# Kernel optimization log

Measured on AMD Instinct MI355X. Metric: run time of the kernel, lower is better.

## Reference

```python
import jax, jax.numpy as jnp
import numpy as np

STATE_LEN = 256
EPS = 1e-5


def _ln(x, g, b):
    m = jnp.mean(x, axis=-1, keepdims=True)
    v = jnp.mean((x - m) ** 2, axis=-1, keepdims=True)
    return (x - m) / jnp.sqrt(v + EPS) * g + b


def setup_inputs() -> dict:
    key = jax.random.key(0)
    ks = jax.random.split(key, 12)
    B, S, L, D, DK, DV = 2, 256, 2048, 512, 64, 64
    T = L + 2 * S  # 2560
    def w(k, i, o):
        return jax.random.normal(k, (i, o), jnp.float32) * 0.02
    return {
        "x": jax.random.normal(ks[0], (B, T, D), jnp.float32),
        "w_q": w(ks[1], D, DK), "w_k": w(ks[2], D, DK), "w_v": w(ks[3], D, DV),
        "w_q_ss": w(ks[4], D, DK), "w_k_ss": w(ks[5], D, DK), "w_v_ss": w(ks[6], D, DV),
        "w_q_se": w(ks[7], D, DK), "w_k_se": w(ks[8], D, DK), "w_v_se": w(ks[9], D, DV),
        "ln_g": jnp.ones((D,), jnp.float32), "ln_b": jnp.zeros((D,), jnp.float32),
        "ln_g_ss": jnp.ones((D,), jnp.float32), "ln_b_ss": jnp.zeros((D,), jnp.float32),
        "ln_g_se": jnp.ones((D,), jnp.float32), "ln_b_se": jnp.zeros((D,), jnp.float32),
        "cope_emb": jax.random.normal(ks[10], (1, DK, T), jnp.float32),
    }


def reference(x, w_q, w_k, w_v, w_q_ss, w_k_ss, w_v_ss, w_q_se, w_k_se, w_v_se,
              ln_g, ln_b, ln_g_ss, ln_b_ss, ln_g_se, ln_b_se, cope_emb):
    S = STATE_LEN
    T = x.shape[1]
    # extract_state: [state_start | main | state_end]
    xs, xm, xe = x[:, :S], x[:, S:T - S], x[:, T - S:]
    xm = _ln(xm, ln_g, ln_b)
    xs = _ln(xs, ln_g_ss, ln_b_ss)
    xe = _ln(xe, ln_g_se, ln_b_se)
    q = jnp.concatenate([xs @ w_q_ss, xm @ w_q, xe @ w_q_se], axis=1)  # [B,T,DK]
    k = jnp.concatenate([xs @ w_k_ss, xm @ w_k, xe @ w_k_se], axis=1)
    v = jnp.concatenate([xs @ w_v_ss, xm @ w_v, xe @ w_v_se], axis=1)
    dk = q.shape[-1]
    # --- CoPE bias ---
    logits = jnp.einsum('btd,bsd->bts', q, k)  # [B,T,T]
    gates = jax.nn.sigmoid(logits)
    # reverse cumsum along keys (flip-cumsum-flip)
    pos = jnp.flip(jnp.cumsum(jnp.flip(gates, -1), axis=-1), -1)
    pos = jnp.minimum(pos, jnp.float32(T - 1))
    pf = jnp.floor(pos)
    pc = jnp.ceil(pos)
    li = jnp.einsum('btd,dm->btm', q, cope_emb[0])  # [B,T,T]
    lc = jnp.take_along_axis(li, pc.astype(jnp.int32), axis=-1)
    lf = jnp.take_along_axis(li, pf.astype(jnp.int32), axis=-1)
    w = pos - pf
    bias = lc * w + lf * (1.0 - w)
    # --- attention with tril-log mask + CoPE bias ---
    causal = jnp.tril(jnp.ones((T, T), dtype=bool))
    att_logits = logits / jnp.sqrt(jnp.float32(dk)) + jnp.where(causal, bias, -jnp.inf)
    attn = jax.nn.softmax(att_logits, axis=-1)
    return jnp.einsum('bts,bsd->btd', attn, v)
```

## Files before the change

### kernel.cpp

```cpp
#include <hip/hip_runtime.h>
#include <hip/hip_bf16.h>
#include <math.h>

using short8 = __attribute__((ext_vector_type(8))) short;
using f32x4  = __attribute__((ext_vector_type(4))) float;

constexpr int S_LEN  = 256;
constexpr int T      = 2560;
constexpr int D_IN   = 512;
constexpr int DK     = 64;
constexpr int B_N    = 2;
constexpr int SS     = 8;

__global__ __launch_bounds__(256) void lnprep_kernel(
    const float* __restrict__ x,
    const float* __restrict__ g_m,  const float* __restrict__ b_m,
    const float* __restrict__ g_s,  const float* __restrict__ b_s,
    const float* __restrict__ g_e,  const float* __restrict__ b_e,
    const float* __restrict__ w_qs, const float* __restrict__ w_ks, const float* __restrict__ w_vs,
    const float* __restrict__ w_q,  const float* __restrict__ w_k,  const float* __restrict__ w_v,
    const float* __restrict__ w_qe, const float* __restrict__ w_ke, const float* __restrict__ w_ve,
    const float* __restrict__ cope,
    __hip_bfloat16* __restrict__ xnh, __hip_bfloat16* __restrict__ xnl,
    __hip_bfloat16* __restrict__ wth, __hip_bfloat16* __restrict__ wtl,
    __hip_bfloat16* __restrict__ copeT)
{
    constexpr int LN_BLOCKS = (B_N * T) / 4;
    if (blockIdx.x < LN_BLOCKS) {
        const int wv   = threadIdx.x >> 6;
        const int lane = threadIdx.x & 63;
        const int row  = blockIdx.x * 4 + wv;
        const int t    = row % T;

        const float *gv, *bv;
        if (t < S_LEN)          { gv = g_s; bv = b_s; }
        else if (t < T - S_LEN) { gv = g_m; bv = b_m; }
        else                    { gv = g_e; bv = b_e; }

        const float4* xr4 = (const float4*)(x + (size_t)row * D_IN);
        float4 a = xr4[lane * 2], b4 = xr4[lane * 2 + 1];
        float xv[8] = {a.x, a.y, a.z, a.w, b4.x, b4.y, b4.z, b4.w};

        float s = 0.f;
#pragma unroll
        for (int j = 0; j < 8; ++j) s += xv[j];
#pragma unroll
        for (int off = 32; off > 0; off >>= 1) s += __shfl_down(s, off);
        s = __shfl(s, 0);
        const float mean = s * (1.0f / D_IN);

        float sq = 0.f;
#pragma unroll
        for (int j = 0; j < 8; ++j) { float d = xv[j] - mean; sq += d * d; }
#pragma unroll
        for (int off = 32; off > 0; off >>= 1) sq += __shfl_down(sq, off);
        sq = __shfl(sq, 0);
        const float inv = rsqrtf(sq * (1.0f / D_IN) + 1e-5f);

        const float4* gv4 = (const float4*)gv;
        const float4* bv4 = (const float4*)bv;
        float4 ga = gv4[lane * 2], gb = gv4[lane * 2 + 1];
        float4 ba = bv4[lane * 2], bb = bv4[lane * 2 + 1];
        float g8[8] = {ga.x, ga.y, ga.z, ga.w, gb.x, gb.y, gb.z, gb.w};
        float b8[8] = {ba.x, ba.y, ba.z, ba.w, bb.x, bb.y, bb.z, bb.w};

        short hs[8], ls[8];
#pragma unroll
        for (int j = 0; j < 8; ++j) {
            float v = (xv[j] - mean) * inv * g8[j] + b8[j];
            __hip_bfloat16 h  = __float2bfloat16(v);
            __hip_bfloat16 lo = __float2bfloat16(v - __bfloat162float(h));
            hs[j] = *(short*)&h;
            ls[j] = *(short*)&lo;
        }
        short8 H = {hs[0],hs[1],hs[2],hs[3],hs[4],hs[5],hs[6],hs[7]};
        short8 L = {ls[0],ls[1],ls[2],ls[3],ls[4],ls[5],ls[6],ls[7]};
        *(short8*)(xnh + (size_t)row * D_IN + lane * 8) = H;
        *(short8*)(xnl + (size_t)row * D_IN + lane * 8) = L;
        return;
    }

    const int i = (blockIdx.x - LN_BLOCKS) * 256 + threadIdx.x;
    constexpr int NW = 9 * DK * D_IN;
    if (i < NW) {
        const int matIdx = i >> 15;
        const int rem = i & 32767;
        const int col = rem >> 9, k = rem & 511;
        const float* W =
            (matIdx == 0) ? w_qs : (matIdx == 1) ? w_ks : (matIdx == 2) ? w_vs :
            (matIdx == 3) ? w_q  : (matIdx == 4) ? w_k  : (matIdx == 5) ? w_v  :
            (matIdx == 6) ? w_qe : (matIdx == 7) ? w_ke : w_ve;
        float f = W[(size_t)k * DK + col];
        __hip_bfloat16 h = __float2bfloat16(f);
        wth[i] = h;
        wtl[i] = __float2bfloat16(f - __bfloat162float(h));
    } else if (i < NW + T * DK) {
        const int j = i - NW;
        const int m = j >> 6, d = j & 63;
        copeT[j] = __float2bfloat16(cope[(size_t)d * T + m]);
    }
}

__global__ __launch_bounds__(256) void qkv_gemm_kernel(
    const __hip_bfloat16* __restrict__ xnh, const __hip_bfloat16* __restrict__ xnl,
    const __hip_bfloat16* __restrict__ wth, const __hip_bfloat16* __restrict__ wtl,
    __hip_bfloat16* __restrict__ qh, __hip_bfloat16* __restrict__ ql,
    __hip_bfloat16* __restrict__ kh, __hip_bfloat16* __restrict__ kl,
    __hip_bfloat16* __restrict__ vT)
{
    const int bid = blockIdx.x;
    const int mt = bid / 3, mat = bid % 3;
    const int r0 = mt * 64;
    const int b  = r0 / T, t0 = r0 % T;
    const int region = (t0 < S_LEN) ? 0 : (t0 < T - S_LEN) ? 1 : 2;
    const int matIdx = region * 3 + mat;

    const int tid = threadIdx.x, lane = tid & 63, wid = tid >> 6;
    const int wm = wid >> 1, wn = wid & 1;
    const int fr = lane & 15, k8 = (lane >> 4) * 8;

    f32x4 acc[2][2];
#pragma unroll
    for (int mf = 0; mf < 2; ++mf)
#pragma unroll
        for (int nf = 0; nf < 2; ++nf) acc[mf][nf] = (f32x4){0.f, 0.f, 0.f, 0.f};

    for (int ks = 0; ks < D_IN / 32; ++ks) {
        const int k = ks * 32 + k8;
        short8 ah[2], al[2], bh2[2], bl2[2];
#pragma unroll
        for (int mf = 0; mf < 2; ++mf) {
            size_t off = (size_t)(r0 + wm * 32 + mf * 16 + fr) * D_IN + k;
            ah[mf] = *(const short8*)(xnh + off);
            al[mf] = *(const short8*)(xnl + off);
        }
#pragma unroll
        for (int nf = 0; nf < 2; ++nf) {
            size_t off = ((size_t)matIdx * DK + wn * 32 + nf * 16 + fr) * D_IN + k;
            bh2[nf] = *(const short8*)(wth + off);
            bl2[nf] = *(const short8*)(wtl + off);
        }
#pragma unroll
        for (int mf = 0; mf < 2; ++mf)
#pragma unroll
            for (int nf = 0; nf < 2; ++nf) {
                acc[mf][nf] = __builtin_amdgcn_mfma_f32_16x16x32_bf16(ah[mf], bh2[nf], acc[mf][nf], 0, 0, 0);
                acc[mf][nf] = __builtin_amdgcn_mfma_f32_16x16x32_bf16(ah[mf], bl2[nf], acc[mf][nf], 0, 0, 0);
                acc[mf][nf] = __builtin_amdgcn_mfma_f32_16x16x32_bf16(al[mf], bh2[nf], acc[mf][nf], 0, 0, 0);
            }
    }

    const int r4 = (lane >> 4) * 4;
#pragma unroll
    for (int mf = 0; mf < 2; ++mf)
#pragma unroll
        for (int nf = 0; nf < 2; ++nf) {
            const int cg = wn * 32 + nf * 16 + fr;
#pragma unroll
            for (int j = 0; j < 4; ++j) {
                const int rg = r0 + wm * 32 + mf * 16 + r4 + j;
                float f = acc[mf][nf][j];
                __hip_bfloat16 h  = __float2bfloat16(f);
                __hip_bfloat16 lo = __float2bfloat16(f - __bfloat162float(h));
                if (mat == 0)      { qh[(size_t)rg * DK + cg] = h; ql[(size_t)rg * DK + cg] = lo; }
                else if (mat == 1) { kh[(size_t)rg * DK + cg] = h; kl[(size_t)rg * DK + cg] = lo; }
                else               { vT[((size_t)b * DK + cg) * T + (rg % T)] = h; }
            }
        }
}

__global__ __launch_bounds__(256) void gemm1_kernel(
    const __hip_bfloat16* __restrict__ qh, const __hip_bfloat16* __restrict__ ql,
    const __hip_bfloat16* __restrict__ kh, const __hip_bfloat16* __restrict__ kl,
    const __hip_bfloat16* __restrict__ copeT,
    float* __restrict__ logc, __hip_bfloat16* __restrict__ lic,
    int b0, int t_off, int TC)
{
    constexpr int TS = T / 64;
    const int per_b = (TC / 128) * TS;
    const int bb  = blockIdx.x / per_b;
    const int rem = blockIdx.x % per_b;
    const int ti  = rem / TS, si = rem % TS;
    const int t0  = ti * 128, s0 = si * 64;
    const int b   = b0 + bb;
    float*          logits_c = logc + (size_t)bb * TC * T;
    __hip_bfloat16* li_c     = lic  + (size_t)bb * TC * T;

    const int tid = threadIdx.x, lane = tid & 63, wid = tid >> 6;
    const int wm  = wid >> 1, wn = wid & 1;
    const int fr  = lane & 15, k8 = (lane >> 4) * 8;
    const size_t qb = (size_t)b * T * DK;

    short8 ah[4][2], al[4][2];
#pragma unroll
    for (int mf = 0; mf < 4; ++mf)
#pragma unroll
        for (int ks = 0; ks < 2; ++ks) {
            size_t off = qb + (size_t)(t_off + t0 + wm * 64 + mf * 16 + fr) * DK + ks * 32 + k8;
            ah[mf][ks] = *(const short8*)(qh + off);
            al[mf][ks] = *(const short8*)(ql + off);
        }
    short8 bh[2][2], bl[2][2], bc[2][2];
#pragma unroll
    for (int nf = 0; nf < 2; ++nf)
#pragma unroll
        for (int ks = 0; ks < 2; ++ks) {
            size_t off = (size_t)(s0 + wn * 32 + nf * 16 + fr) * DK + ks * 32 + k8;
            bh[nf][ks] = *(const short8*)(kh + qb + off);
            bl[nf][ks] = *(const short8*)(kl + qb + off);
            bc[nf][ks] = *(const short8*)(copeT + off);
        }

    f32x4 accL[4][2], accM[4][2];
#pragma unroll
    for (int mf = 0; mf < 4; ++mf)
#pragma unroll
        for (int nf = 0; nf < 2; ++nf) {
            accL[mf][nf] = (f32x4){0.f, 0.f, 0.f, 0.f};
            accM[mf][nf] = (f32x4){0.f, 0.f, 0.f, 0.f};
        }

#pragma unroll
    for (int mf = 0; mf < 4; ++mf)
#pragma unroll
        for (int nf = 0; nf < 2; ++nf)
#pragma unroll
            for (int ks = 0; ks < 2; ++ks) {
                accL[mf][nf] = __builtin_amdgcn_mfma_f32_16x16x32_bf16(ah[mf][ks], bh[nf][ks], accL[mf][nf], 0, 0, 0);
                accL[mf][nf] = __builtin_amdgcn_mfma_f32_16x16x32_bf16(ah[mf][ks], bl[nf][ks], accL[mf][nf], 0, 0, 0);
                accL[mf][nf] = __builtin_amdgcn_mfma_f32_16x16x32_bf16(al[mf][ks], bh[nf][ks], accL[mf][nf], 0, 0, 0);
                accM[mf][nf] = __builtin_amdgcn_mfma_f32_16x16x32_bf16(ah[mf][ks], bc[nf][ks], accM[mf][nf], 0, 0, 0);
            }

    const int r4 = (lane >> 4) * 4;
#pragma unroll
    for (int mf = 0; mf < 4; ++mf)
#pragma unroll
        for (int nf = 0; nf < 2; ++nf) {
            const int cg = s0 + wn * 32 + nf * 16 + fr;
#pragma unroll
            for (int j = 0; j < 4; ++j) {
                const int rl = t0 + wm * 64 + mf * 16 + r4 + j;
                const size_t o = (size_t)rl * T + cg;
                logits_c[o] = accL[mf][nf][j];
                li_c[o]     = __float2bfloat16(accM[mf][nf][j]);
            }
        }
}

__global__ __launch_bounds__(256) void phase2_kernel(
    const float* __restrict__ logc, __hip_bfloat16* __restrict__ lic,
    int t_off, int TC)
{
    constexpr int CH = T / 256;
    const int tid  = threadIdx.x;
    const int lane = tid & 63;
    const int wv   = tid >> 6;
    const int bb   = blockIdx.x / TC;
    const int rl   = blockIdx.x % TC;
    const int t    = t_off + rl;

    __shared__ __hip_bfloat16 sli[T];
    __shared__ float redS[4], redM[4], redE[4];

    const float*    lrow  = logc + ((size_t)bb * TC + rl) * T;
    __hip_bfloat16* lirow = lic  + ((size_t)bb * TC + rl) * T;

#pragma unroll
    for (int i = 0; i < 5; ++i) {
        const int idx = i * 256 + tid;
        ((unsigned int*)sli)[idx] = ((const unsigned int*)lirow)[idx];
    }

    const int s0 = tid * CH;
    float lg[CH], g[CH];
    float lsum = 0.f;
    const float2* lr2 = (const float2*)(lrow + s0);
#pragma unroll
    for (int i = 0; i < 5; ++i) {
        float2 v = lr2[i];
        lg[2 * i] = v.x; lg[2 * i + 1] = v.y;
    }
#pragma unroll
    for (int i = 0; i < CH; ++i) {
        g[i] = 1.0f / (1.0f + __expf(-lg[i]));
        lsum += g[i];
    }

    float incl = lsum;
#pragma unroll
    for (int off = 1; off < 64; off <<= 1) {
        float n = __shfl_up(incl, off);
        if (lane >= off) incl += n;
    }
    if (lane == 63) redS[wv] = incl;
    __syncthreads();
    float total = 0.f, wpre = 0.f;
#pragma unroll
    for (int w2 = 0; w2 < 4; ++w2) {
        float tw = redS[w2];
        total += tw;
        if (w2 < wv) wpre += tw;
    }
    float run = wpre + incl - lsum;

    float att[CH];
    float lmax = -INFINITY;
#pragma unroll
    for (int i = 0; i < CH; ++i) {
        int s = s0 + i;
        float pos = total - run;
        run += g[i];
        pos = fminf(pos, (float)(T - 1));
        float pf = floorf(pos);
        float w  = pos - pf;
        int ipf  = (int)pf;
        int ipc  = (int)ceilf(pos);
        float bias = __bfloat162float(sli[ipc]) * w
                   + __bfloat162float(sli[ipf]) * (1.0f - w);
        float al = lg[i] * 0.125f + bias;
        if (s > t) al = -INFINITY;
        att[i] = al;
        lmax = fmaxf(lmax, al);
    }

#pragma unroll
    for (int off = 32; off > 0; off >>= 1) lmax = fmaxf(lmax, __shfl_down(lmax, off));
    if (lane == 0) redM[wv] = lmax;
    __syncthreads();
    const float bmax = fmaxf(fmaxf(redM[0], redM[1]), fmaxf(redM[2], redM[3]));

    float e[CH];
    float esum = 0.f;
#pragma unroll
    for (int i = 0; i < CH; ++i) {
        e[i] = __expf(att[i] - bmax);
        esum += e[i];
    }
#pragma unroll
    for (int off = 32; off > 0; off >>= 1) esum += __shfl_down(esum, off);
    if (lane == 0) redE[wv] = esum;
    __syncthreads();
    const float rden = 1.0f / (redE[0] + redE[1] + redE[2] + redE[3]);

    unsigned int pw[5];
#pragma unroll
    for (int i = 0; i < 5; ++i) {
        __hip_bfloat16 p0 = __float2bfloat16(e[2 * i] * rden);
        __hip_bfloat16 p1 = __float2bfloat16(e[2 * i + 1] * rden);
        pw[i] = (unsigned int)*(unsigned short*)&p0
              | ((unsigned int)*(unsigned short*)&p1 << 16);
    }
    unsigned int* dst = (unsigned int*)(lirow + s0);
#pragma unroll
    for (int i = 0; i < 5; ++i) dst[i] = pw[i];
}

__global__ __launch_bounds__(256) void gemm2_kernel(
    const __hip_bfloat16* __restrict__ lic, const __hip_bfloat16* __restrict__ vT,
    float* __restrict__ part, int b0, int t_off, int TC)
{
    const int per_b = (TC / 128) * SS;
    const int bb  = blockIdx.x / per_b;
    const int rem = blockIdx.x % per_b;
    const int ti  = rem / SS, sc = rem % SS;
    const int t0  = ti * 128;
    const int sb  = sc * (T / SS);
    if (sb > t_off + t0 + 127) return;
    const int b   = b0 + bb;
    const __hip_bfloat16* p_c = lic + (size_t)bb * TC * T;

    const int tid = threadIdx.x, lane = tid & 63, wid = tid >> 6;
    const int wm  = wid >> 1, wn = wid & 1;
    const int fr  = lane & 15, k8 = (lane >> 4) * 8;
    const size_t vb = (size_t)b * DK * T;

    f32x4 acc[4][2];
#pragma unroll
    for (int mf = 0; mf < 4; ++mf)
#pragma unroll
        for (int nf = 0; nf < 2; ++nf) acc[mf][nf] = (f32x4){0.f, 0.f, 0.f, 0.f};

    for (int ks = 0; ks < (T / SS) / 32; ++ks) {
        const int s = sb + ks * 32 + k8;
        short8 a_p[4], bv[2];
#pragma unroll
        for (int mf = 0; mf < 4; ++mf)
            a_p[mf] = *(const short8*)(p_c + (size_t)(t0 + wm * 64 + mf * 16 + fr) * T + s);
#pragma unroll
        for (int nf = 0; nf < 2; ++nf)
            bv[nf] = *(const short8*)(vT + vb + (size_t)(wn * 32 + nf * 16 + fr) * T + s);
#pragma unroll
        for (int mf = 0; mf < 4; ++mf)
#pragma unroll
            for (int nf = 0; nf < 2; ++nf)
                acc[mf][nf] = __builtin_amdgcn_mfma_f32_16x16x32_bf16(a_p[mf], bv[nf], acc[mf][nf], 0, 0, 0);
    }

    const int r4 = (lane >> 4) * 4;
#pragma unroll
    for (int mf = 0; mf < 4; ++mf)
#pragma unroll
        for (int nf = 0; nf < 2; ++nf) {
            const int cg = wn * 32 + nf * 16 + fr;
#pragma unroll
            for (int j = 0; j < 4; ++j) {
                const int rl = t0 + wm * 64 + mf * 16 + r4 + j;
                part[(((size_t)bb * SS + sc) * TC + rl) * DK + cg] = acc[mf][nf][j];
            }
        }
}

__global__ __launch_bounds__(256) void reduce_kernel(
    const float* __restrict__ part, float* __restrict__ out,
    int b0, int t_off, int TC)
{
    const int per_b = (TC * DK) / 256;
    const int bb = blockIdx.x / per_b;
    const int ii = (blockIdx.x % per_b) * 256 + threadIdx.x;
    const int rl = ii >> 6, d = ii & 63;
    const int t  = t_off + rl;
    const int sc_max = min(SS - 1, t / (T / SS));
    float s = 0.f;
    for (int sc = 0; sc <= sc_max; ++sc)
        s += part[(((size_t)bb * SS + sc) * TC + rl) * DK + d];
    out[((size_t)(b0 + bb) * T + t) * DK + d] = s;
}

extern "C" void kernel_launch(void* const* d_in, const int* in_sizes, int n_in,
                              void* d_out, int out_size, void* d_ws, size_t ws_size,
                              hipStream_t stream)
{
    const float* x    = (const float*)d_in[0];
    const float* w_q  = (const float*)d_in[1];
    const float* w_k  = (const float*)d_in[2];
    const float* w_v  = (const float*)d_in[3];
    const float* w_qs = (const float*)d_in[4];
    const float* w_ks = (const float*)d_in[5];
    const float* w_vs = (const float*)d_in[6];
    const float* w_qe = (const float*)d_in[7];
    const float* w_ke = (const float*)d_in[8];
    const float* w_ve = (const float*)d_in[9];
    const float* g_m  = (const float*)d_in[10];
    const float* b_m  = (const float*)d_in[11];
    const float* g_s  = (const float*)d_in[12];
    const float* b_s  = (const float*)d_in[13];
    const float* g_e  = (const float*)d_in[14];
    const float* b_e  = (const float*)d_in[15];
    const float* cope = (const float*)d_in[16];

    const size_t n_qk  = (size_t)B_N * T * DK;
    const size_t n_xn  = (size_t)B_N * T * D_IN;
    const size_t n_wt  = (size_t)9 * DK * D_IN;
    const size_t fixedB = 5 * n_qk * 2 + (size_t)T * DK * 2
                        + 2 * n_xn * 2 + 2 * n_wt * 2;
    auto chunkB = [&](size_t TC) -> size_t {
        return TC * (size_t)T * 4
             + TC * (size_t)T * 2
             + (size_t)SS * TC * DK * 4;
    };
    int TC, NB;
    if (fixedB + 2 * chunkB(T) <= ws_size)       { TC = T;    NB = 2; }
    else if (fixedB + chunkB(T) <= ws_size)      { TC = T;    NB = 1; }
    else if (fixedB + chunkB(1280) <= ws_size)   { TC = 1280; NB = 1; }
    else                                         { TC = 640;  NB = 1; }

    char* w = (char*)d_ws;
    __hip_bfloat16* qh    = (__hip_bfloat16*)w; w += n_qk * 2;
    __hip_bfloat16* ql    = (__hip_bfloat16*)w; w += n_qk * 2;
    __hip_bfloat16* kh    = (__hip_bfloat16*)w; w += n_qk * 2;
    __hip_bfloat16* kl    = (__hip_bfloat16*)w; w += n_qk * 2;
    __hip_bfloat16* vT    = (__hip_bfloat16*)w; w += n_qk * 2;
    __hip_bfloat16* copeT = (__hip_bfloat16*)w; w += (size_t)T * DK * 2;
    __hip_bfloat16* xnh   = (__hip_bfloat16*)w; w += n_xn * 2;
    __hip_bfloat16* xnl   = (__hip_bfloat16*)w; w += n_xn * 2;
    __hip_bfloat16* wth   = (__hip_bfloat16*)w; w += n_wt * 2;
    __hip_bfloat16* wtl   = (__hip_bfloat16*)w; w += n_wt * 2;
    float*          logc  = (float*)w;          w += (size_t)NB * TC * T * 4;
    __hip_bfloat16* lic   = (__hip_bfloat16*)w; w += (size_t)NB * TC * T * 2;
    float*          part  = (float*)w;

    constexpr int LN_BLOCKS   = (B_N * T) / 4;
    const int     PREP_BLOCKS = (int)((n_wt + (size_t)T * DK + 255) / 256);
    lnprep_kernel<<<LN_BLOCKS + PREP_BLOCKS, 256, 0, stream>>>(
        x, g_m, b_m, g_s, b_s, g_e, b_e,
        w_qs, w_ks, w_vs, w_q, w_k, w_v, w_qe, w_ke, w_ve, cope,
        xnh, xnl, wth, wtl, copeT);

    qkv_gemm_kernel<<<(B_N * T / 64) * 3, 256, 0, stream>>>(
        xnh, xnl, wth, wtl, qh, ql, kh, kl, vT);

    for (int b0 = 0; b0 < B_N; b0 += NB)
        for (int t_off = 0; t_off < T; t_off += TC) {
            gemm1_kernel<<<NB * (TC / 128) * (T / 64), 256, 0, stream>>>(
                qh, ql, kh, kl, copeT, logc, lic, b0, t_off, TC);
            phase2_kernel<<<NB * TC, 256, 0, stream>>>(
                logc, lic, t_off, TC);
            gemm2_kernel<<<NB * (TC / 128) * SS, 256, 0, stream>>>(
                lic, vT, part, b0, t_off, TC);
            reduce_kernel<<<NB * (TC * DK) / 256, 256, 0, stream>>>(
                part, (float*)d_out, b0, t_off, TC);
        }
}
```

Baseline: 105.6 us.

## Fuse LayerNorm into QKV projection GEMM via swizzled shared-memory tiles

LayerNorm is now computed inside the QKV projection kernel. Each block normalizes its 32 rows, splits them into bf16 hi/lo halves, stores those in XOR-swizzled LDS, and runs the MFMA GEMM from LDS. This removes the global round-trip of the normalized activations (two bf16 copies of B*T*D) and one dependent phase between launches. In exchange, each row is normalized three times (once per Q/K/V block), the row tile shrinks from 64 to 32, and 64KB of LDS per block limits occupancy.

```diff
diff --git a/kernel.cpp b/kernel.cpp
--- a/kernel.cpp
+++ b/kernel.cpp
@@ -12,75 +12,15 @@
 constexpr int B_N    = 2;
 constexpr int SS     = 8;
 
-__global__ __launch_bounds__(256) void lnprep_kernel(
-    const float* __restrict__ x,
-    const float* __restrict__ g_m,  const float* __restrict__ b_m,
-    const float* __restrict__ g_s,  const float* __restrict__ b_s,
-    const float* __restrict__ g_e,  const float* __restrict__ b_e,
+__global__ __launch_bounds__(256) void prep_kernel(
     const float* __restrict__ w_qs, const float* __restrict__ w_ks, const float* __restrict__ w_vs,
     const float* __restrict__ w_q,  const float* __restrict__ w_k,  const float* __restrict__ w_v,
     const float* __restrict__ w_qe, const float* __restrict__ w_ke, const float* __restrict__ w_ve,
     const float* __restrict__ cope,
-    __hip_bfloat16* __restrict__ xnh, __hip_bfloat16* __restrict__ xnl,
     __hip_bfloat16* __restrict__ wth, __hip_bfloat16* __restrict__ wtl,
     __hip_bfloat16* __restrict__ copeT)
 {
-    constexpr int LN_BLOCKS = (B_N * T) / 4;
-    if (blockIdx.x < LN_BLOCKS) {
-        const int wv   = threadIdx.x >> 6;
-        const int lane = threadIdx.x & 63;
-        const int row  = blockIdx.x * 4 + wv;
-        const int t    = row % T;
-
-        const float *gv, *bv;
-        if (t < S_LEN)          { gv = g_s; bv = b_s; }
-        else if (t < T - S_LEN) { gv = g_m; bv = b_m; }
-        else                    { gv = g_e; bv = b_e; }
-
-        const float4* xr4 = (const float4*)(x + (size_t)row * D_IN);
-        float4 a = xr4[lane * 2], b4 = xr4[lane * 2 + 1];
-        float xv[8] = {a.x, a.y, a.z, a.w, b4.x, b4.y, b4.z, b4.w};
-
-        float s = 0.f;
-#pragma unroll
-        for (int j = 0; j < 8; ++j) s += xv[j];
-#pragma unroll
-        for (int off = 32; off > 0; off >>= 1) s += __shfl_down(s, off);
-        s = __shfl(s, 0);
-        const float mean = s * (1.0f / D_IN);
-
-        float sq = 0.f;
-#pragma unroll
-        for (int j = 0; j < 8; ++j) { float d = xv[j] - mean; sq += d * d; }
-#pragma unroll
-        for (int off = 32; off > 0; off >>= 1) sq += __shfl_down(sq, off);
-        sq = __shfl(sq, 0);
-        const float inv = rsqrtf(sq * (1.0f / D_IN) + 1e-5f);
-
-        const float4* gv4 = (const float4*)gv;
-        const float4* bv4 = (const float4*)bv;
-        float4 ga = gv4[lane * 2], gb = gv4[lane * 2 + 1];
-        float4 ba = bv4[lane * 2], bb = bv4[lane * 2 + 1];
-        float g8[8] = {ga.x, ga.y, ga.z, ga.w, gb.x, gb.y, gb.z, gb.w};
-        float b8[8] = {ba.x, ba.y, ba.z, ba.w, bb.x, bb.y, bb.z, bb.w};
-
-        short hs[8], ls[8];
-#pragma unroll
-        for (int j = 0; j < 8; ++j) {
-            float v = (xv[j] - mean) * inv * g8[j] + b8[j];
-            __hip_bfloat16 h  = __float2bfloat16(v);
-            __hip_bfloat16 lo = __float2bfloat16(v - __bfloat162float(h));
-            hs[j] = *(short*)&h;
-            ls[j] = *(short*)&lo;
-        }
-        short8 H = {hs[0],hs[1],hs[2],hs[3],hs[4],hs[5],hs[6],hs[7]};
-        short8 L = {ls[0],ls[1],ls[2],ls[3],ls[4],ls[5],ls[6],ls[7]};
-        *(short8*)(xnh + (size_t)row * D_IN + lane * 8) = H;
-        *(short8*)(xnl + (size_t)row * D_IN + lane * 8) = L;
-        return;
-    }
-
-    const int i = (blockIdx.x - LN_BLOCKS) * 256 + threadIdx.x;
+    const int i = blockIdx.x * 256 + threadIdx.x;
     constexpr int NW = 9 * DK * D_IN;
     if (i < NW) {
         const int matIdx = i >> 15;
@@ -101,72 +41,121 @@
     }
 }
 
-__global__ __launch_bounds__(256) void qkv_gemm_kernel(
-    const __hip_bfloat16* __restrict__ xnh, const __hip_bfloat16* __restrict__ xnl,
+__global__ __launch_bounds__(256) void lnqkv_kernel(
+    const float* __restrict__ x,
+    const float* __restrict__ g_m,  const float* __restrict__ b_m,
+    const float* __restrict__ g_s,  const float* __restrict__ b_s,
+    const float* __restrict__ g_e,  const float* __restrict__ b_e,
     const __hip_bfloat16* __restrict__ wth, const __hip_bfloat16* __restrict__ wtl,
     __hip_bfloat16* __restrict__ qh, __hip_bfloat16* __restrict__ ql,
     __hip_bfloat16* __restrict__ kh, __hip_bfloat16* __restrict__ kl,
     __hip_bfloat16* __restrict__ vT)
 {
+    __shared__ __align__(16) char lxh[32 * 1024];
+    __shared__ __align__(16) char lxl[32 * 1024];
+
     const int bid = blockIdx.x;
     const int mt = bid / 3, mat = bid % 3;
-    const int r0 = mt * 64;
+    const int r0 = mt * 32;
     const int b  = r0 / T, t0 = r0 % T;
     const int region = (t0 < S_LEN) ? 0 : (t0 < T - S_LEN) ? 1 : 2;
     const int matIdx = region * 3 + mat;
 
     const int tid = threadIdx.x, lane = tid & 63, wid = tid >> 6;
+
+    const float *gv, *bv;
+    if (region == 0)      { gv = g_s; bv = b_s; }
+    else if (region == 1) { gv = g_m; bv = b_m; }
+    else                  { gv = g_e; bv = b_e; }
+
+    const float4* gv4 = (const float4*)gv;
+    const float4* bv4 = (const float4*)bv;
+    float4 ga = gv4[lane * 2], gb = gv4[lane * 2 + 1];
+    float4 ba = bv4[lane * 2], bb = bv4[lane * 2 + 1];
+    float g8[8] = {ga.x, ga.y, ga.z, ga.w, gb.x, gb.y, gb.z, gb.w};
+    float b8[8] = {ba.x, ba.y, ba.z, ba.w, bb.x, bb.y, bb.z, bb.w};
+
+    for (int r8 = 0; r8 < 8; ++r8) {
+        const int row  = wid * 8 + r8;
+        const int grow = r0 + row;
+        const float4* xr4 = (const float4*)(x + (size_t)grow * D_IN);
+        float4 a = xr4[lane * 2], b4 = xr4[lane * 2 + 1];
+        float xv[8] = {a.x, a.y, a.z, a.w, b4.x, b4.y, b4.z, b4.w};
+
+        float s = 0.f;
+#pragma unroll
+        for (int j = 0; j < 8; ++j) s += xv[j];
+#pragma unroll
+        for (int off = 32; off > 0; off >>= 1) s += __shfl_down(s, off);
+        s = __shfl(s, 0);
+        const float mean = s * (1.0f / D_IN);
+
+        float sq = 0.f;
+#pragma unroll
+        for (int j = 0; j < 8; ++j) { float d = xv[j] - mean; sq += d * d; }
+#pragma unroll
+        for (int off = 32; off > 0; off >>= 1) sq += __shfl_down(sq, off);
+        sq = __shfl(sq, 0);
+        const float inv = rsqrtf(sq * (1.0f / D_IN) + 1e-5f);
+
+        short hs[8], ls[8];
+#pragma unroll
+        for (int j = 0; j < 8; ++j) {
+            float v = (xv[j] - mean) * inv * g8[j] + b8[j];
+            __hip_bfloat16 h  = __float2bfloat16(v);
+            __hip_bfloat16 lo = __float2bfloat16(v - __bfloat162float(h));
+            hs[j] = *(short*)&h;
+            ls[j] = *(short*)&lo;
+        }
+        short8 H = {hs[0],hs[1],hs[2],hs[3],hs[4],hs[5],hs[6],hs[7]};
+        short8 L = {ls[0],ls[1],ls[2],ls[3],ls[4],ls[5],ls[6],ls[7]};
+        const int boff = row * 1024 + ((lane * 16) ^ ((row & 7) << 4));
+        *(short8*)(lxh + boff) = H;
+        *(short8*)(lxl + boff) = L;
+    }
+    __syncthreads();
+
     const int wm = wid >> 1, wn = wid & 1;
-    const int fr = lane & 15, k8 = (lane >> 4) * 8;
-
-    f32x4 acc[2][2];
-#pragma unroll
-    for (int mf = 0; mf < 2; ++mf)
-#pragma unroll
-        for (int nf = 0; nf < 2; ++nf) acc[mf][nf] = (f32x4){0.f, 0.f, 0.f, 0.f};
+    const int fr = lane & 15;
+    const int arow  = wm * 16 + fr;
+    const int abase = arow * 1024;
+    const int aswz  = (arow & 7) << 4;
+
+    f32x4 acc[2];
+    acc[0] = (f32x4){0.f, 0.f, 0.f, 0.f};
+    acc[1] = (f32x4){0.f, 0.f, 0.f, 0.f};
 
     for (int ks = 0; ks < D_IN / 32; ++ks) {
-        const int k = ks * 32 + k8;
-        short8 ah[2], al[2], bh2[2], bl2[2];
-#pragma unroll
-        for (int mf = 0; mf < 2; ++mf) {
-            size_t off = (size_t)(r0 + wm * 32 + mf * 16 + fr) * D_IN + k;
-            ah[mf] = *(const short8*)(xnh + off);
-            al[mf] = *(const short8*)(xnl + off);
-        }
+        const int bc = ks * 64 + (lane >> 4) * 16;
+        short8 ahv = *(const short8*)(lxh + abase + (bc ^ aswz));
+        short8 alv = *(const short8*)(lxl + abase + (bc ^ aswz));
+        const int k = ks * 32 + (lane >> 4) * 8;
 #pragma unroll
         for (int nf = 0; nf < 2; ++nf) {
             size_t off = ((size_t)matIdx * DK + wn * 32 + nf * 16 + fr) * D_IN + k;
-            bh2[nf] = *(const short8*)(wth + off);
-            bl2[nf] = *(const short8*)(wtl + off);
-        }
-#pragma unroll
-        for (int mf = 0; mf < 2; ++mf)
-#pragma unroll
-            for (int nf = 0; nf < 2; ++nf) {
-                acc[mf][nf] = __builtin_amdgcn_mfma_f32_16x16x32_bf16(ah[mf], bh2[nf], acc[mf][nf], 0, 0, 0);
-                acc[mf][nf] = __builtin_amdgcn_mfma_f32_16x16x32_bf16(ah[mf], bl2[nf], acc[mf][nf], 0, 0, 0);
-                acc[mf][nf] = __builtin_amdgcn_mfma_f32_16x16x32_bf16(al[mf], bh2[nf], acc[mf][nf], 0, 0, 0);
-            }
+            short8 bh2 = *(const short8*)(wth + off);
+            short8 bl2 = *(const short8*)(wtl + off);
+            acc[nf] = __builtin_amdgcn_mfma_f32_16x16x32_bf16(ahv, bh2, acc[nf], 0, 0, 0);
+            acc[nf] = __builtin_amdgcn_mfma_f32_16x16x32_bf16(ahv, bl2, acc[nf], 0, 0, 0);
+            acc[nf] = __builtin_amdgcn_mfma_f32_16x16x32_bf16(alv, bh2, acc[nf], 0, 0, 0);
+        }
     }
 
     const int r4 = (lane >> 4) * 4;
 #pragma unroll
-    for (int mf = 0; mf < 2; ++mf)
-#pragma unroll
-        for (int nf = 0; nf < 2; ++nf) {
-            const int cg = wn * 32 + nf * 16 + fr;
-#pragma unroll
-            for (int j = 0; j < 4; ++j) {
-                const int rg = r0 + wm * 32 + mf * 16 + r4 + j;
-                float f = acc[mf][nf][j];
-                __hip_bfloat16 h  = __float2bfloat16(f);
-                __hip_bfloat16 lo = __float2bfloat16(f - __bfloat162float(h));
-                if (mat == 0)      { qh[(size_t)rg * DK + cg] = h; ql[(size_t)rg * DK + cg] = lo; }
-                else if (mat == 1) { kh[(size_t)rg * DK + cg] = h; kl[(size_t)rg * DK + cg] = lo; }
-                else               { vT[((size_t)b * DK + cg) * T + (rg % T)] = h; }
-            }
-        }
+    for (int nf = 0; nf < 2; ++nf) {
+        const int cg = wn * 32 + nf * 16 + fr;
+#pragma unroll
+        for (int j = 0; j < 4; ++j) {
+            const int rg = r0 + wm * 16 + r4 + j;
+            float f = acc[nf][j];
+            __hip_bfloat16 h  = __float2bfloat16(f);
+            __hip_bfloat16 lo = __float2bfloat16(f - __bfloat162float(h));
+            if (mat == 0)      { qh[(size_t)rg * DK + cg] = h; ql[(size_t)rg * DK + cg] = lo; }
+            else if (mat == 1) { kh[(size_t)rg * DK + cg] = h; kl[(size_t)rg * DK + cg] = lo; }
+            else               { vT[((size_t)b * DK + cg) * T + (rg % T)] = h; }
+        }
+    }
 }
 
 __global__ __launch_bounds__(256) void gemm1_kernel(
@@ -450,10 +439,8 @@
     const float* cope = (const float*)d_in[16];
 
     const size_t n_qk  = (size_t)B_N * T * DK;
-    const size_t n_xn  = (size_t)B_N * T * D_IN;
     const size_t n_wt  = (size_t)9 * DK * D_IN;
-    const size_t fixedB = 5 * n_qk * 2 + (size_t)T * DK * 2
-                        + 2 * n_xn * 2 + 2 * n_wt * 2;
+    const size_t fixedB = 5 * n_qk * 2 + (size_t)T * DK * 2 + 2 * n_wt * 2;
     auto chunkB = [&](size_t TC) -> size_t {
         return TC * (size_t)T * 4
              + TC * (size_t)T * 2
@@ -472,23 +459,20 @@
     __hip_bfloat16* kl    = (__hip_bfloat16*)w; w += n_qk * 2;
     __hip_bfloat16* vT    = (__hip_bfloat16*)w; w += n_qk * 2;
     __hip_bfloat16* copeT = (__hip_bfloat16*)w; w += (size_t)T * DK * 2;
-    __hip_bfloat16* xnh   = (__hip_bfloat16*)w; w += n_xn * 2;
-    __hip_bfloat16* xnl   = (__hip_bfloat16*)w; w += n_xn * 2;
     __hip_bfloat16* wth   = (__hip_bfloat16*)w; w += n_wt * 2;
     __hip_bfloat16* wtl   = (__hip_bfloat16*)w; w += n_wt * 2;
     float*          logc  = (float*)w;          w += (size_t)NB * TC * T * 4;
     __hip_bfloat16* lic   = (__hip_bfloat16*)w; w += (size_t)NB * TC * T * 2;
     float*          part  = (float*)w;
 
-    constexpr int LN_BLOCKS   = (B_N * T) / 4;
-    const int     PREP_BLOCKS = (int)((n_wt + (size_t)T * DK + 255) / 256);
-    lnprep_kernel<<<LN_BLOCKS + PREP_BLOCKS, 256, 0, stream>>>(
-        x, g_m, b_m, g_s, b_s, g_e, b_e,
+    constexpr int NW = 9 * DK * D_IN;
+    prep_kernel<<<(NW + T * DK + 255) / 256, 256, 0, stream>>>(
         w_qs, w_ks, w_vs, w_q, w_k, w_v, w_qe, w_ke, w_ve, cope,
-        xnh, xnl, wth, wtl, copeT);
-
-    qkv_gemm_kernel<<<(B_N * T / 64) * 3, 256, 0, stream>>>(
-        xnh, xnl, wth, wtl, qh, ql, kh, kl, vT);
+        wth, wtl, copeT);
+
+    lnqkv_kernel<<<(B_N * T / 32) * 3, 256, 0, stream>>>(
+        x, g_m, b_m, g_s, b_s, g_e, b_e, wth, wtl,
+        qh, ql, kh, kl, vT);
 
     for (int b0 = 0; b0 < B_N; b0 += NB)
         for (int t_off = 0; t_off < T; t_off += TC) {
```

Result: no change. 107.5 us (+1.8%).
